# Kernel tuning notes

Measured on AMD Instinct MI355X. Metric: run time of the kernel, lower is better.

Reference implementation:

```python
import jax, jax.numpy as jnp
import numpy as np

N, L, S, D, HD, FC = 4, 2048, 2048, 256, 256, 8  # batch, query len, source len, in_depth, hidden_depth, heads
EPS = 1e-12  # F.normalize eps


def setup_inputs() -> dict:
    key = jax.random.key(0)
    ks = jax.random.split(key, 8)
    sc = 0.05
    return {
        "x0": jax.random.normal(ks[0], (N, L, D), jnp.float32),
        "x1": jax.random.normal(ks[1], (N, S, D), jnp.float32),
        "W0": jax.random.normal(ks[2], (D, HD), jnp.float32) * sc,
        "b0": jax.random.normal(ks[3], (HD,), jnp.float32) * sc,
        "W1": jax.random.normal(ks[4], (D, 2 * HD), jnp.float32) * sc,
        "b1": jax.random.normal(ks[5], (2 * HD,), jnp.float32) * sc,
        "Wm": jax.random.normal(ks[6], (HD, D), jnp.float32) * sc,
        "bm": jax.random.normal(ks[7], (D,), jnp.float32) * sc,
        "alpha": jnp.ones((1,), jnp.float32),
        "beta": jnp.zeros((1,), jnp.float32),
    }


def _l2norm(x):
    # F.normalize(dim=2): x / max(||x||, eps)
    return x / jnp.maximum(jnp.linalg.norm(x, axis=2, keepdims=True), EPS)


def reference(x0, x1, W0, b0, W1, b1, Wm, bm, alpha, beta):
    n, l, _ = x0.shape
    s = x1.shape[1]
    fc = FC
    m = n * fc
    # projections + head split: 'n l (fc c) -> (n fc) l c'
    x0p = (x0 @ W0 + b0).reshape(n, l, fc, -1).transpose(0, 2, 1, 3).reshape(m, l, -1)
    x1p = (x1 @ W1 + b1).reshape(n, s, fc, -1).transpose(0, 2, 1, 3).reshape(m, s, -1)
    x1_point, x1_value = jnp.split(x1p, 2, axis=2)  # each (m, s, c)
    # cosine similarity (m, l, s)
    sim = jnp.einsum('mlc,msc->mls', _l2norm(x0p), _l2norm(x1_point))
    sim = jax.nn.sigmoid(alpha * sim + beta)
    max_val = jnp.max(sim, axis=2)              # (m, l)
    max_idx = jnp.argmax(sim, axis=2)           # (m, l)
    gathered = jnp.take_along_axis(x1_value, max_idx[:, :, None], axis=1)  # (m, l, c)
    new_x0 = max_val[:, :, None] * gathered
    # '(n fc) l c -> n l (fc c)'
    new_x0 = new_x0.reshape(n, fc, l, -1).transpose(0, 2, 1, 3).reshape(n, l, -1)
    return new_x0 @ Wm + bm
```

## Files before the change

kernel.cpp:

```cpp
#include <hip/hip_runtime.h>
#include <hip/hip_bf16.h>
#include <cmath>

#define NB   4
#define LQ   2048
#define SK   2048
#define DD   256
#define HD   256
#define FC   8
#define CH   32
#define MHEAD 32

#define MARGIN 0.0085f
#define CAP    16

#define KROW 40

typedef float f32x16 __attribute__((ext_vector_type(16)));
typedef float f32x2  __attribute__((ext_vector_type(2)));
typedef short bf16x8 __attribute__((ext_vector_type(8)));
typedef unsigned short ushort8v __attribute__((ext_vector_type(8)));

__device__ inline unsigned short f32_to_bf16_bits(float v) {
    __hip_bfloat16 b = __float2bfloat16(v);
    return __builtin_bit_cast(unsigned short, b);
}
__device__ inline unsigned int ord_encode(float v) {
    unsigned int u = __float_as_uint(v);
    return (u & 0x80000000u) ? ~u : (u | 0x80000000u);
}
__device__ inline float ord_decode(unsigned int e) {
    unsigned int u = (e & 0x80000000u) ? (e & 0x7fffffffu) : ~e;
    return __uint_as_float(u);
}

#define MFMA32(a, b, c) __builtin_amdgcn_mfma_f32_32x32x16_bf16(a, b, c, 0, 0, 0)

__global__ __launch_bounds__(256, 7)
void proj_gemm_kernel(const float* __restrict__ x0, const float* __restrict__ x1,
                      const float* __restrict__ W0, const float* __restrict__ b0f,
                      const float* __restrict__ W1, const float* __restrict__ b1f,
                      float* __restrict__ xq, float* __restrict__ xk)
{
    __shared__ float As[2][16][68];
    __shared__ float Bs[2][16][64];
    const int nt  = blockIdx.x;
    const bool is0 = (nt < 4);
    const float* A    = is0 ? x0 : x1;
    const float* B    = is0 ? W0 : W1;
    const float* bias = is0 ? b0f : b1f;
    float* dst        = is0 ? xq : xk;
    const int NB_ = is0 ? HD : 2 * HD;
    const int hw  = is0 ? 32 : 64;
    const int bm  = blockIdx.y * 64;
    const int K   = DD;

    const int tx = threadIdx.x & 15;
    const int ty = threadIdx.x >> 4;
    f32x2 acc2[4][2] = {};

    const int arow = threadIdx.x >> 2;
    const int akq  = (threadIdx.x & 3) << 2;
    const int bkr  = threadIdx.x >> 4;
    const int bnq  = (threadIdx.x & 15) << 2;
    const int fl   = (nt & 3) * 2 + (bnq >> 5);
    const int bcol = fl * hw + (bnq & 31);

    {
        const float4 a4 = *(const float4*)&A[(size_t)(bm + arow) * K + akq];
        const float4 b4 = *(const float4*)&B[(size_t)bkr * NB_ + bcol];
        As[0][akq + 0][arow] = a4.x;
        As[0][akq + 1][arow] = a4.y;
        As[0][akq + 2][arow] = a4.z;
        As[0][akq + 3][arow] = a4.w;
        *(float4*)&Bs[0][bkr][bnq] = b4;
    }
    __syncthreads();

    const int nchunk = K >> 4;
    float4 pa, pb;
    for (int c = 0; c < nchunk; ++c) {
        const int cur = c & 1;
        if (c + 1 < nchunk) {
            const int k0 = (c + 1) << 4;
            pa = *(const float4*)&A[(size_t)(bm + arow) * K + k0 + akq];
            pb = *(const float4*)&B[(size_t)(k0 + bkr) * NB_ + bcol];
        }
        #pragma unroll
        for (int kk = 0; kk < 16; ++kk) {
            const float4 a4 = *(const float4*)&As[cur][kk][ty << 2];
            const float4 bv = *(const float4*)&Bs[cur][kk][tx << 2];
            const f32x2 b01 = {bv.x, bv.y};
            const f32x2 b23 = {bv.z, bv.w};
            const float av[4] = {a4.x, a4.y, a4.z, a4.w};
            #pragma unroll
            for (int i = 0; i < 4; ++i) {
                const f32x2 aa = {av[i], av[i]};
                acc2[i][0] = __builtin_elementwise_fma(aa, b01, acc2[i][0]);
                acc2[i][1] = __builtin_elementwise_fma(aa, b23, acc2[i][1]);
            }
        }
        if (c + 1 < nchunk) {
            const int nxt = cur ^ 1;
            As[nxt][akq + 0][arow] = pa.x;
            As[nxt][akq + 1][arow] = pa.y;
            As[nxt][akq + 2][arow] = pa.z;
            As[nxt][akq + 3][arow] = pa.w;
            *(float4*)&Bs[nxt][bkr][bnq] = pb;
        }
        __syncthreads();
    }

    #pragma unroll
    for (int i = 0; i < 4; ++i) {
        const int row = bm + (ty << 2) + i;
        const int n = row >> 11, l = row & 2047;
        #pragma unroll
        for (int j = 0; j < 4; ++j) {
            const int cl = (tx << 2) + j;
            const int f  = (nt & 3) * 2 + (cl >> 5);
            const int cc = cl & 31;
            const float v = acc2[i][j >> 1][j & 1] + bias[f * hw + cc];
            dst[((((size_t)n * FC + f) * LQ) + l) * CH + cc] = v;
        }
    }
}

__global__ __launch_bounds__(256)
void prep_kernel(const float* __restrict__ x1, const float* __restrict__ Wm,
                 const float* __restrict__ W1,
                 unsigned short* __restrict__ x1b,
                 unsigned short* __restrict__ wm_s,
                 unsigned short* __restrict__ wv_s)
{
    const int i = blockIdx.x * 256 + threadIdx.x;
    if (i < 262144) {
        const float4 a = *(const float4*)(x1 + (size_t)i * 8);
        const float4 b = *(const float4*)(x1 + (size_t)i * 8 + 4);
        ushort8v o;
        o[0] = f32_to_bf16_bits(a.x); o[1] = f32_to_bf16_bits(a.y);
        o[2] = f32_to_bf16_bits(a.z); o[3] = f32_to_bf16_bits(a.w);
        o[4] = f32_to_bf16_bits(b.x); o[5] = f32_to_bf16_bits(b.y);
        o[6] = f32_to_bf16_bits(b.z); o[7] = f32_to_bf16_bits(b.w);
        *(ushort8v*)(x1b + (size_t)i * 8) = o;
    } else if (i < 262144 + 65536) {
        const int j = i - 262144;
        const int k = j >> 8, n = j & 255;
        wm_s[(k >> 4) * 4096 + n * 16 + (k & 15)] = f32_to_bf16_bits(Wm[k * 256 + n]);
    } else {
        const int j = i - 327680;
        const int k = j >> 8, v = j & 255;
        const int w = (v >> 5) * 64 + 32 + (v & 31);
        wv_s[(k >> 4) * 4096 + v * 16 + (k & 15)] = f32_to_bf16_bits(W1[k * 512 + w]);
    }
}

__global__ __launch_bounds__(256)
void val_gemm_kernel(const unsigned short* __restrict__ x1b,
                     const unsigned short* __restrict__ wv_s,
                     const float* __restrict__ b1f, float* __restrict__ xv)
{
    const int wave = threadIdx.x >> 6;
    const int lane = threadIdx.x & 63;
    const int idx  = blockIdx.x * 4 + wave;
    const int mt   = idx >> 3;
    const int nt   = idx & 7;
    const int col  = lane & 31;
    const int g8   = (lane >> 5) * 8;

    const unsigned short* aptr = x1b + (size_t)(mt * 32 + col) * 256 + g8;
    const unsigned short* bptr = wv_s + nt * 32 * 16 + col * 16 + g8;

    f32x16 acc = {0.f, 0.f, 0.f, 0.f, 0.f, 0.f, 0.f, 0.f,
                  0.f, 0.f, 0.f, 0.f, 0.f, 0.f, 0.f, 0.f};
    #pragma unroll 4
    for (int kc = 0; kc < 16; ++kc) {
        const bf16x8 a = *(const bf16x8*)(aptr + kc * 16);
        const bf16x8 bfr = *(const bf16x8*)(bptr + (size_t)kc * 4096);
        acc = MFMA32(a, bfr, acc);
    }

    const int v = nt * 32 + col;
    const int f = v >> 5, c = v & 31;
    const float bias = b1f[f * 64 + 32 + c];
    #pragma unroll
    for (int r = 0; r < 16; ++r) {
        const int g = mt * 32 + (r & 3) + 8 * (r >> 2) + 4 * (lane >> 5);
        const int n = g >> 11, s = g & 2047;
        xv[((((size_t)n * FC + f) * SK) + s) * CH + c] = acc[r] + bias;
    }
}

__global__ __launch_bounds__(256)
void norm_split_init_kernel(float* __restrict__ xq, unsigned short* __restrict__ qhi,
                            float* __restrict__ xk, unsigned short* __restrict__ khi,
                            const float* __restrict__ alpha,
                            unsigned int* __restrict__ maxhh_u, int* __restrict__ cnt)
{
    int r = blockIdx.x * blockDim.x + threadIdx.x;
    float* p;
    unsigned short* dhi;
    float sgn = 1.f;
    if (r < MHEAD * LQ) {
        maxhh_u[r] = 0u;
        cnt[r] = 0;
        p   = xq + (size_t)r * CH;
        dhi = qhi + (size_t)r * CH;
        if (alpha[0] < 0.f) sgn = -1.f;
    } else {
        r -= MHEAD * LQ;
        p   = xk + (size_t)r * CH;
        dhi = khi + (size_t)r * CH;
    }

    float4 v[8];
    float ss = 0.f;
    #pragma unroll
    for (int i = 0; i < 8; ++i) {
        v[i] = *(const float4*)(p + i * 4);
        ss = fmaf(v[i].x, v[i].x, ss);
        ss = fmaf(v[i].y, v[i].y, ss);
        ss = fmaf(v[i].z, v[i].z, ss);
        ss = fmaf(v[i].w, v[i].w, ss);
    }
    const float inv = sgn / fmaxf(sqrtf(ss), 1e-12f);

    ushort8v hb[4];
    #pragma unroll
    for (int i = 0; i < 8; ++i) {
        float4 w;
        w.x = v[i].x * inv; w.y = v[i].y * inv;
        w.z = v[i].z * inv; w.w = v[i].w * inv;
        *(float4*)(p + i * 4) = w;
        hb[i >> 1][(i & 1) * 4 + 0] = f32_to_bf16_bits(w.x);
        hb[i >> 1][(i & 1) * 4 + 1] = f32_to_bf16_bits(w.y);
        hb[i >> 1][(i & 1) * 4 + 2] = f32_to_bf16_bits(w.z);
        hb[i >> 1][(i & 1) * 4 + 3] = f32_to_bf16_bits(w.w);
    }
    #pragma unroll
    for (int i = 0; i < 4; ++i)
        *(ushort8v*)(dhi + i * 8) = hb[i];
}

__global__ __launch_bounds__(256, 4)
void maxpass_kernel(const unsigned short* __restrict__ qhi,
                    const unsigned short* __restrict__ khi,
                    unsigned int* __restrict__ maxhh_u)
{
    __shared__ unsigned short kbuf[2][128 * KROW];
    const int b    = blockIdx.x;
    const int sc   = b & 3;
    const int qb   = (b >> 2) & 15;
    const int h    = b >> 6;
    const int wave = threadIdx.x >> 6;
    const int lane = threadIdx.x & 63;
    const int t    = threadIdx.x;
    const int qbase = qb * 128 + wave * 32;
    const int col   = lane & 31;
    const int g8    = (lane >> 5) * 8;

    const size_t qoff = ((size_t)h * LQ + qbase + col) * CH + g8;
    const bf16x8 ah0 = *(const bf16x8*)(qhi + qoff);
    const bf16x8 ah1 = *(const bf16x8*)(qhi + qoff + 16);

    const unsigned short* kh = khi + ((size_t)h * SK + sc * 512) * CH;

    const int srow  = t >> 1;
    const int shalf = (t & 1) * 16;
    const unsigned short* sp = kh + (size_t)srow * CH + shalf;

    float maxv[16];
    #pragma unroll
    for (int r = 0; r < 16; ++r) maxv[r] = -INFINITY;

    bf16x8 s0 = *(const bf16x8*)(sp);
    bf16x8 s1 = *(const bf16x8*)(sp + 8);
    *(bf16x8*)(&kbuf[0][srow * KROW + shalf])     = s0;
    *(bf16x8*)(&kbuf[0][srow * KROW + shalf + 8]) = s1;
    __syncthreads();

    for (int g = 0; g < 4; ++g) {
        if (g < 3) {
            const unsigned short* spn = sp + (size_t)(g + 1) * 128 * CH;
            s0 = *(const bf16x8*)(spn);
            s1 = *(const bf16x8*)(spn + 8);
        }
        const unsigned short* kbp = &kbuf[g & 1][0];
        #pragma unroll
        for (int tt = 0; tt < 4; ++tt) {
            const int rl = tt * 32 + col;
            const bf16x8 ka  = *(const bf16x8*)(kbp + rl * KROW + g8);
            const bf16x8 kbv = *(const bf16x8*)(kbp + rl * KROW + 16 + g8);
            f32x16 c = {0.f, 0.f, 0.f, 0.f, 0.f, 0.f, 0.f, 0.f,
                        0.f, 0.f, 0.f, 0.f, 0.f, 0.f, 0.f, 0.f};
            c = MFMA32(ah0, ka, c);
            c = MFMA32(ah1, kbv, c);
            #pragma unroll
            for (int r = 0; r < 16; ++r) maxv[r] = fmaxf(maxv[r], c[r]);
        }
        if (g < 3) {
            unsigned short* swn = &kbuf[(g + 1) & 1][srow * KROW + shalf];
            *(bf16x8*)(swn)     = s0;
            *(bf16x8*)(swn + 8) = s1;
            __syncthreads();
        }
    }

    #pragma unroll
    for (int r = 0; r < 16; ++r) {
        float v = maxv[r];
        #pragma unroll
        for (int m = 16; m >= 1; m >>= 1)
            v = fmaxf(v, __shfl_xor(v, m, 64));
        maxv[r] = v;
    }
    if (col == 0) {
        const int rbase = h * LQ + qbase + 4 * (lane >> 5);
        #pragma unroll
        for (int r = 0; r < 16; ++r)
            atomicMax(&maxhh_u[rbase + (r & 3) + 8 * (r >> 2)], ord_encode(maxv[r]));
    }
}

__global__ __launch_bounds__(256, 4)
void candpass_kernel(const unsigned short* __restrict__ qhi,
                     const unsigned short* __restrict__ khi,
                     const unsigned int* __restrict__ maxhh_u,
                     int* __restrict__ cnt, int* __restrict__ cand)
{
    __shared__ unsigned short kbuf[2][128 * KROW];
    const int b    = blockIdx.x;
    const int sc   = b & 3;
    const int qb   = (b >> 2) & 15;
    const int h    = b >> 6;
    const int wave = threadIdx.x >> 6;
    const int lane = threadIdx.x & 63;
    const int t    = threadIdx.x;
    const int qbase = qb * 128 + wave * 32;
    const int col   = lane & 31;
    const int g8    = (lane >> 5) * 8;

    const size_t qoff = ((size_t)h * LQ + qbase + col) * CH + g8;
    const bf16x8 ah0 = *(const bf16x8*)(qhi + qoff);
    const bf16x8 ah1 = *(const bf16x8*)(qhi + qoff + 16);

    int   rows[16];
    float thr[16];
    {
        const int rbase = h * LQ + qbase + 4 * (lane >> 5);
        #pragma unroll
        for (int r = 0; r < 16; ++r) {
            rows[r] = rbase + (r & 3) + 8 * (r >> 2);
            thr[r]  = ord_decode(maxhh_u[rows[r]]) - MARGIN;
        }
    }

    const unsigned short* kh = khi + ((size_t)h * SK + sc * 512) * CH;
    const int sbase = sc * 512;

    const int srow  = t >> 1;
    const int shalf = (t & 1) * 16;
    const unsigned short* sp = kh + (size_t)srow * CH + shalf;

    bf16x8 s0 = *(const bf16x8*)(sp);
    bf16x8 s1 = *(const bf16x8*)(sp + 8);
    *(bf16x8*)(&kbuf[0][srow * KROW + shalf])     = s0;
    *(bf16x8*)(&kbuf[0][srow * KROW + shalf + 8]) = s1;
    __syncthreads();

    for (int g = 0; g < 4; ++g) {
        if (g < 3) {
            const unsigned short* spn = sp + (size_t)(g + 1) * 128 * CH;
            s0 = *(const bf16x8*)(spn);
            s1 = *(const bf16x8*)(spn + 8);
        }
        const unsigned short* kbp = &kbuf[g & 1][0];
        #pragma unroll
        for (int tt = 0; tt < 4; ++tt) {
            const int rl = tt * 32 + col;
            const bf16x8 ka  = *(const bf16x8*)(kbp + rl * KROW + g8);
            const bf16x8 kbv = *(const bf16x8*)(kbp + rl * KROW + 16 + g8);
            f32x16 c = {0.f, 0.f, 0.f, 0.f, 0.f, 0.f, 0.f, 0.f,
                        0.f, 0.f, 0.f, 0.f, 0.f, 0.f, 0.f, 0.f};
            c = MFMA32(ah0, ka, c);
            c = MFMA32(ah1, kbv, c);

            unsigned int hit = 0u;
            #pragma unroll
            for (int r = 0; r < 16; ++r)
                hit = (c[r] >= thr[r]) ? (hit | (1u << r)) : hit;
            if (hit) {
                const int s = sbase + g * 128 + tt * 32 + col;
                #pragma unroll
                for (int r = 0; r < 16; ++r) {
                    if (hit & (1u << r)) {
                        const int slot = atomicAdd(&cnt[rows[r]], 1);
                        if (slot < CAP) cand[(size_t)rows[r] * CAP + slot] = s;
                    }
                }
            }
        }
        if (g < 3) {
            unsigned short* swn = &kbuf[(g + 1) & 1][srow * KROW + shalf];
            *(bf16x8*)(swn)     = s0;
            *(bf16x8*)(swn + 8) = s1;
            __syncthreads();
        }
    }
}

__global__ __launch_bounds__(256)
void refine_gather_kernel(const float* __restrict__ qn,
                          const float* __restrict__ kn,
                          const int* __restrict__ cnt, const int* __restrict__ cand,
                          const float* __restrict__ xv,
                          const float* __restrict__ alpha, const float* __restrict__ beta,
                          unsigned short* __restrict__ nxb)
{
    const int r = blockIdx.x * blockDim.x + threadIdx.x;
    const int h = r >> 11, l = r & 2047;

    float qr[CH];
    #pragma unroll
    for (int i = 0; i < 8; ++i) {
        const float4 v = *(const float4*)(qn + (size_t)r * CH + i * 4);
        qr[i * 4 + 0] = v.x; qr[i * 4 + 1] = v.y;
        qr[i * 4 + 2] = v.z; qr[i * 4 + 3] = v.w;
    }

    int m = cnt[r];
    if (m > CAP) m = CAP;
    float best = -INFINITY;
    int   bidx = 0x7fffffff;
    for (int j = 0; j < m; ++j) {
        const int s = cand[(size_t)r * CAP + j];
        const float4* k4 = (const float4*)(kn + ((size_t)h * SK + s) * CH);
        float p = 0.f;
        #pragma unroll
        for (int c = 0; c < 8; ++c) {
            const float4 kv = k4[c];
            p = fmaf(qr[c * 4 + 0], kv.x, p);
            p = fmaf(qr[c * 4 + 1], kv.y, p);
            p = fmaf(qr[c * 4 + 2], kv.z, p);
            p = fmaf(qr[c * 4 + 3], kv.w, p);
        }
        if (p > best || (p == best && s < bidx)) { best = p; bidx = s; }
    }
    if (bidx == 0x7fffffff) bidx = 0;

    const float a = alpha[0], be = beta[0];
    float tv;
    int idx = bidx;
    if (a == 0.f) { idx = 0; tv = be; }
    else          { tv = fmaf(fabsf(a), best, be); }
    float val;
    if (tv >= 0.f) val = 1.f / (1.f + expf(-tv));
    else           { const float e = expf(tv); val = e / (1.f + e); }

    const float4* vr = (const float4*)(xv + ((size_t)h * SK + idx) * CH);
    const int n = h >> 3, f = h & 7;
    unsigned short* out = nxb + (((size_t)n * LQ + l) * (FC * CH)) + f * CH;
    #pragma unroll
    for (int i = 0; i < 8; ++i) {
        const float4 w = vr[i];
        ushort8v o;
        o[0] = f32_to_bf16_bits(w.x * val);
        o[1] = f32_to_bf16_bits(w.y * val);
        o[2] = f32_to_bf16_bits(w.z * val);
        o[3] = f32_to_bf16_bits(w.w * val);
        *(unsigned long long*)(out + i * 4) = __builtin_bit_cast(unsigned long long,
            *(const ulong1*)&o);
    }
}

__global__ __launch_bounds__(256)
void gemm_out_mfma_kernel(const unsigned short* __restrict__ nxb,
                          const unsigned short* __restrict__ wm_s,
                          const float* __restrict__ bm, float* __restrict__ out)
{
    const int wave = threadIdx.x >> 6;
    const int lane = threadIdx.x & 63;
    const int idx  = blockIdx.x * 4 + wave;
    const int mt   = idx >> 3;
    const int nt   = idx & 7;
    const int col  = lane & 31;
    const int g8   = (lane >> 5) * 8;

    const unsigned short* aptr = nxb + (size_t)(mt * 32 + col) * 256 + g8;
    const unsigned short* bptr = wm_s + nt * 32 * 16 + col * 16 + g8;

    f32x16 acc = {0.f, 0.f, 0.f, 0.f, 0.f, 0.f, 0.f, 0.f,
                  0.f, 0.f, 0.f, 0.f, 0.f, 0.f, 0.f, 0.f};
    #pragma unroll 4
    for (int kc = 0; kc < 16; ++kc) {
        const bf16x8 a = *(const bf16x8*)(aptr + kc * 16);
        const bf16x8 bfr = *(const bf16x8*)(bptr + (size_t)kc * 4096);
        acc = MFMA32(a, bfr, acc);
    }

    const int n0 = nt * 32;
    const float bias = bm[n0 + col];
    #pragma unroll
    for (int r = 0; r < 16; ++r) {
        const int row = mt * 32 + (r & 3) + 8 * (r >> 2) + 4 * (lane >> 5);
        out[(size_t)row * 256 + n0 + col] = acc[r] + bias;
    }
}

extern "C" void kernel_launch(void* const* d_in, const int* in_sizes, int n_in,
                              void* d_out, int out_size, void* d_ws, size_t ws_size,
                              hipStream_t stream)
{
    const float* x0 = (const float*)d_in[0];
    const float* x1 = (const float*)d_in[1];
    const float* W0 = (const float*)d_in[2];
    const float* b0 = (const float*)d_in[3];
    const float* W1 = (const float*)d_in[4];
    const float* b1 = (const float*)d_in[5];
    const float* Wm = (const float*)d_in[6];
    const float* bm = (const float*)d_in[7];
    const float* alpha = (const float*)d_in[8];
    const float* beta  = (const float*)d_in[9];
    float* out = (float*)d_out;

    char* ws = (char*)d_ws;
    const size_t MB = 1024ull * 1024ull;
    float* x0q = (float*)(ws + 0);
    float* x1k = (float*)(ws + 8 * MB);
    float* x1v = (float*)(ws + 16 * MB);
    unsigned short* qhi = (unsigned short*)(ws + 24 * MB);
    unsigned short* khi = (unsigned short*)(ws + 28 * MB);
    unsigned short* x1b = (unsigned short*)(ws + 32 * MB);
    int* cand = (int*)(ws + 32 * MB);
    unsigned int* maxhh_u = (unsigned int*)(ws + 36 * MB);
    int* cnt  = (int*)(ws + 36 * MB + 256 * 1024);
    unsigned short* wm_s = (unsigned short*)(ws + 36 * MB + 512 * 1024);
    unsigned short* wv_s = (unsigned short*)(ws + 36 * MB + 640 * 1024);
    unsigned short* nxb  = (unsigned short*)(ws + 24 * MB);

    const int Mrows = NB * LQ;

    proj_gemm_kernel<<<dim3(8, Mrows / 64), 256, 0, stream>>>(
        x0, x1, W0, b0, W1, b1, x0q, x1k);
    prep_kernel<<<1536, 256, 0, stream>>>(x1, Wm, W1, x1b, wm_s, wv_s);
    val_gemm_kernel<<<512, 256, 0, stream>>>(x1b, wv_s, b1, x1v);
    norm_split_init_kernel<<<(2 * MHEAD * LQ) / 256, 256, 0, stream>>>(
        x0q, qhi, x1k, khi, alpha, maxhh_u, cnt);
    maxpass_kernel<<<2048, 256, 0, stream>>>(qhi, khi, maxhh_u);
    candpass_kernel<<<2048, 256, 0, stream>>>(qhi, khi, maxhh_u, cnt, cand);
    refine_gather_kernel<<<(MHEAD * LQ) / 256, 256, 0, stream>>>(
        x0q, x1k, cnt, cand, x1v, alpha, beta, nxb);
    gemm_out_mfma_kernel<<<512, 256, 0, stream>>>(nxb, wm_s, bm, out);
}
```

Measured before the change: 134.8 us.

## Fuse L2-normalization into projection GEMM epilogue and enlarge max/cand blocks

Removes the separate norm_split_init kernel. The projection GEMM now stages its output tile in shared memory and normalizes each 32-wide head row in the epilogue, writing both the fp32 and bf16 copies. The maxhh/cnt zeroing moves into prep_kernel. maxpass and candpass switch to 512-thread blocks covering 256 queries each, so every K tile loaded to LDS is reused by twice as many waves. The costs are a serialized epilogue in which only 128 threads do the normalization, and a larger shared/register footprint per block.

```diff
diff --git a/kernel.cpp b/kernel.cpp
--- a/kernel.cpp
+++ b/kernel.cpp
@@ -40,16 +40,20 @@
 void proj_gemm_kernel(const float* __restrict__ x0, const float* __restrict__ x1,
                       const float* __restrict__ W0, const float* __restrict__ b0f,
                       const float* __restrict__ W1, const float* __restrict__ b1f,
-                      float* __restrict__ xq, float* __restrict__ xk)
-{
-    __shared__ float As[2][16][68];
-    __shared__ float Bs[2][16][64];
+                      const float* __restrict__ alpha,
+                      float* __restrict__ xq, float* __restrict__ xk,
+                      unsigned short* __restrict__ qhi, unsigned short* __restrict__ khi)
+{
+    __shared__ float SH[4224];
+    #define AS(bf,k,m) SH[(bf)*1088 + (k)*68 + (m)]
+    #define BS(bf,k,n) SH[2176 + (bf)*1024 + (k)*64 + (n)]
     const int nt  = blockIdx.x;
     const bool is0 = (nt < 4);
     const float* A    = is0 ? x0 : x1;
     const float* B    = is0 ? W0 : W1;
     const float* bias = is0 ? b0f : b1f;
-    float* dst        = is0 ? xq : xk;
+    float* dst              = is0 ? xq : xk;
+    unsigned short* dhi     = is0 ? qhi : khi;
     const int NB_ = is0 ? HD : 2 * HD;
     const int hw  = is0 ? 32 : 64;
     const int bm  = blockIdx.y * 64;
@@ -69,11 +73,11 @@
     {
         const float4 a4 = *(const float4*)&A[(size_t)(bm + arow) * K + akq];
         const float4 b4 = *(const float4*)&B[(size_t)bkr * NB_ + bcol];
-        As[0][akq + 0][arow] = a4.x;
-        As[0][akq + 1][arow] = a4.y;
-        As[0][akq + 2][arow] = a4.z;
-        As[0][akq + 3][arow] = a4.w;
-        *(float4*)&Bs[0][bkr][bnq] = b4;
+        AS(0, akq + 0, arow) = a4.x;
+        AS(0, akq + 1, arow) = a4.y;
+        AS(0, akq + 2, arow) = a4.z;
+        AS(0, akq + 3, arow) = a4.w;
+        *(float4*)&BS(0, bkr, bnq) = b4;
     }
     __syncthreads();
 
@@ -88,8 +92,8 @@
         }
         #pragma unroll
         for (int kk = 0; kk < 16; ++kk) {
-            const float4 a4 = *(const float4*)&As[cur][kk][ty << 2];
-            const float4 bv = *(const float4*)&Bs[cur][kk][tx << 2];
+            const float4 a4 = *(const float4*)&AS(cur, kk, ty << 2);
+            const float4 bv = *(const float4*)&BS(cur, kk, tx << 2);
             const f32x2 b01 = {bv.x, bv.y};
             const f32x2 b23 = {bv.z, bv.w};
             const float av[4] = {a4.x, a4.y, a4.z, a4.w};
@@ -102,28 +106,66 @@
         }
         if (c + 1 < nchunk) {
             const int nxt = cur ^ 1;
-            As[nxt][akq + 0][arow] = pa.x;
-            As[nxt][akq + 1][arow] = pa.y;
-            As[nxt][akq + 2][arow] = pa.z;
-            As[nxt][akq + 3][arow] = pa.w;
-            *(float4*)&Bs[nxt][bkr][bnq] = pb;
+            AS(nxt, akq + 0, arow) = pa.x;
+            AS(nxt, akq + 1, arow) = pa.y;
+            AS(nxt, akq + 2, arow) = pa.z;
+            AS(nxt, akq + 3, arow) = pa.w;
+            *(float4*)&BS(nxt, bkr, bnq) = pb;
         }
         __syncthreads();
     }
 
     #pragma unroll
     for (int i = 0; i < 4; ++i) {
-        const int row = bm + (ty << 2) + i;
-        const int n = row >> 11, l = row & 2047;
+        const int row = (ty << 2) + i;
         #pragma unroll
         for (int j = 0; j < 4; ++j) {
             const int cl = (tx << 2) + j;
             const int f  = (nt & 3) * 2 + (cl >> 5);
-            const int cc = cl & 31;
-            const float v = acc2[i][j >> 1][j & 1] + bias[f * hw + cc];
-            dst[((((size_t)n * FC + f) * LQ) + l) * CH + cc] = v;
-        }
-    }
+            SH[row * 66 + cl] = acc2[i][j >> 1][j & 1] + bias[f * hw + (cl & 31)];
+        }
+    }
+    __syncthreads();
+    if (threadIdx.x < 128) {
+        const int row  = threadIdx.x >> 1;
+        const int half = threadIdx.x & 1;
+        const float* src = SH + row * 66 + half * 32;
+        float x[32];
+        float ss = 0.f;
+        #pragma unroll
+        for (int c = 0; c < 32; ++c) {
+            x[c] = src[c];
+            ss = fmaf(x[c], x[c], ss);
+        }
+        float sgn = 1.f;
+        if (is0 && alpha[0] < 0.f) sgn = -1.f;
+        const float inv = sgn / fmaxf(sqrtf(ss), 1e-12f);
+        const int grow = bm + row;
+        const int n = grow >> 11, l = grow & 2047;
+        const int f = (nt & 3) * 2 + half;
+        const size_t off = ((((size_t)n * FC + f) * LQ) + l) * CH;
+        float* df = dst + off;
+        unsigned short* dh = dhi + off;
+        #pragma unroll
+        for (int c4 = 0; c4 < 8; ++c4) {
+            float4 w;
+            w.x = x[c4 * 4 + 0] * inv;
+            w.y = x[c4 * 4 + 1] * inv;
+            w.z = x[c4 * 4 + 2] * inv;
+            w.w = x[c4 * 4 + 3] * inv;
+            *(float4*)(df + c4 * 4) = w;
+        }
+        #pragma unroll
+        for (int c8 = 0; c8 < 4; ++c8) {
+            ushort8v o;
+            #pragma unroll
+            for (int j = 0; j < 8; ++j)
+                o[j] = f32_to_bf16_bits(x[c8 * 8 + j] * inv);
+            *(ushort8v*)(dh + c8 * 8) = o;
+        }
+    }
+    #undef AS
+    #undef BS
 }
 
 __global__ __launch_bounds__(256)
@@ -131,7 +173,8 @@
                  const float* __restrict__ W1,
                  unsigned short* __restrict__ x1b,
                  unsigned short* __restrict__ wm_s,
-                 unsigned short* __restrict__ wv_s)
+                 unsigned short* __restrict__ wv_s,
+                 unsigned int* __restrict__ maxhh_u, int* __restrict__ cnt)
 {
     const int i = blockIdx.x * 256 + threadIdx.x;
     if (i < 262144) {
@@ -143,15 +186,19 @@
         o[4] = f32_to_bf16_bits(b.x); o[5] = f32_to_bf16_bits(b.y);
         o[6] = f32_to_bf16_bits(b.z); o[7] = f32_to_bf16_bits(b.w);
         *(ushort8v*)(x1b + (size_t)i * 8) = o;
-    } else if (i < 262144 + 65536) {
+    } else if (i < 327680) {
         const int j = i - 262144;
         const int k = j >> 8, n = j & 255;
         wm_s[(k >> 4) * 4096 + n * 16 + (k & 15)] = f32_to_bf16_bits(Wm[k * 256 + n]);
-    } else {
+    } else if (i < 393216) {
         const int j = i - 327680;
         const int k = j >> 8, v = j & 255;
         const int w = (v >> 5) * 64 + 32 + (v & 31);
         wv_s[(k >> 4) * 4096 + v * 16 + (k & 15)] = f32_to_bf16_bits(W1[k * 512 + w]);
+    } else if (i < 458752) {
+        maxhh_u[i - 393216] = 0u;
+    } else {
+        cnt[i - 458752] = 0;
     }
 }
 
@@ -191,58 +238,7 @@
     }
 }
 
-__global__ __launch_bounds__(256)
-void norm_split_init_kernel(float* __restrict__ xq, unsigned short* __restrict__ qhi,
-                            float* __restrict__ xk, unsigned short* __restrict__ khi,
-                            const float* __restrict__ alpha,
-                            unsigned int* __restrict__ maxhh_u, int* __restrict__ cnt)
-{
-    int r = blockIdx.x * blockDim.x + threadIdx.x;
-    float* p;
-    unsigned short* dhi;
-    float sgn = 1.f;
-    if (r < MHEAD * LQ) {
-        maxhh_u[r] = 0u;
-        cnt[r] = 0;
-        p   = xq + (size_t)r * CH;
-        dhi = qhi + (size_t)r * CH;
-        if (alpha[0] < 0.f) sgn = -1.f;
-    } else {
-        r -= MHEAD * LQ;
-        p   = xk + (size_t)r * CH;
-        dhi = khi + (size_t)r * CH;
-    }
-
-    float4 v[8];
-    float ss = 0.f;
-    #pragma unroll
-    for (int i = 0; i < 8; ++i) {
-        v[i] = *(const float4*)(p + i * 4);
-        ss = fmaf(v[i].x, v[i].x, ss);
-        ss = fmaf(v[i].y, v[i].y, ss);
-        ss = fmaf(v[i].z, v[i].z, ss);
-        ss = fmaf(v[i].w, v[i].w, ss);
-    }
-    const float inv = sgn / fmaxf(sqrtf(ss), 1e-12f);
-
-    ushort8v hb[4];
-    #pragma unroll
-    for (int i = 0; i < 8; ++i) {
-        float4 w;
-        w.x = v[i].x * inv; w.y = v[i].y * inv;
-        w.z = v[i].z * inv; w.w = v[i].w * inv;
-        *(float4*)(p + i * 4) = w;
-        hb[i >> 1][(i & 1) * 4 + 0] = f32_to_bf16_bits(w.x);
-        hb[i >> 1][(i & 1) * 4 + 1] = f32_to_bf16_bits(w.y);
-        hb[i >> 1][(i & 1) * 4 + 2] = f32_to_bf16_bits(w.z);
-        hb[i >> 1][(i & 1) * 4 + 3] = f32_to_bf16_bits(w.w);
-    }
-    #pragma unroll
-    for (int i = 0; i < 4; ++i)
-        *(ushort8v*)(dhi + i * 8) = hb[i];
-}
-
-__global__ __launch_bounds__(256, 4)
+__global__ __launch_bounds__(512, 4)
 void maxpass_kernel(const unsigned short* __restrict__ qhi,
                     const unsigned short* __restrict__ khi,
                     unsigned int* __restrict__ maxhh_u)
@@ -250,12 +246,12 @@
     __shared__ unsigned short kbuf[2][128 * KROW];
     const int b    = blockIdx.x;
     const int sc   = b & 3;
-    const int qb   = (b >> 2) & 15;
-    const int h    = b >> 6;
-    const int wave = threadIdx.x >> 6;
-    const int lane = threadIdx.x & 63;
+    const int qb   = (b >> 2) & 7;
+    const int h    = b >> 5;
     const int t    = threadIdx.x;
-    const int qbase = qb * 128 + wave * 32;
+    const int wave = t >> 6;
+    const int lane = t & 63;
+    const int qbase = qb * 256 + wave * 32;
     const int col   = lane & 31;
     const int g8    = (lane >> 5) * 8;
 
@@ -265,26 +261,20 @@
 
     const unsigned short* kh = khi + ((size_t)h * SK + sc * 512) * CH;
 
-    const int srow  = t >> 1;
-    const int shalf = (t & 1) * 16;
-    const unsigned short* sp = kh + (size_t)srow * CH + shalf;
+    const int srow = t >> 2;
+    const int sq   = (t & 3) * 8;
+    const unsigned short* sp = kh + (size_t)srow * CH + sq;
 
     float maxv[16];
     #pragma unroll
     for (int r = 0; r < 16; ++r) maxv[r] = -INFINITY;
 
     bf16x8 s0 = *(const bf16x8*)(sp);
-    bf16x8 s1 = *(const bf16x8*)(sp + 8);
-    *(bf16x8*)(&kbuf[0][srow * KROW + shalf])     = s0;
-    *(bf16x8*)(&kbuf[0][srow * KROW + shalf + 8]) = s1;
+    *(bf16x8*)(&kbuf[0][srow * KROW + sq]) = s0;
     __syncthreads();
 
     for (int g = 0; g < 4; ++g) {
-        if (g < 3) {
-            const unsigned short* spn = sp + (size_t)(g + 1) * 128 * CH;
-            s0 = *(const bf16x8*)(spn);
-            s1 = *(const bf16x8*)(spn + 8);
-        }
+        if (g < 3) s0 = *(const bf16x8*)(sp + (size_t)(g + 1) * 128 * CH);
         const unsigned short* kbp = &kbuf[g & 1][0];
         #pragma unroll
         for (int tt = 0; tt < 4; ++tt) {
@@ -299,9 +289,7 @@
             for (int r = 0; r < 16; ++r) maxv[r] = fmaxf(maxv[r], c[r]);
         }
         if (g < 3) {
-            unsigned short* swn = &kbuf[(g + 1) & 1][srow * KROW + shalf];
-            *(bf16x8*)(swn)     = s0;
-            *(bf16x8*)(swn + 8) = s1;
+            *(bf16x8*)(&kbuf[(g + 1) & 1][srow * KROW + sq]) = s0;
             __syncthreads();
         }
     }
@@ -322,7 +310,7 @@
     }
 }
 
-__global__ __launch_bounds__(256, 4)
+__global__ __launch_bounds__(512, 4)
 void candpass_kernel(const unsigned short* __restrict__ qhi,
                      const unsigned short* __restrict__ khi,
                      const unsigned int* __restrict__ maxhh_u,
@@ -331,12 +319,12 @@
     __shared__ unsigned short kbuf[2][128 * KROW];
     const int b    = blockIdx.x;
     const int sc   = b & 3;
-    const int qb   = (b >> 2) & 15;
-    const int h    = b >> 6;
-    const int wave = threadIdx.x >> 6;
-    const int lane = threadIdx.x & 63;
+    const int qb   = (b >> 2) & 7;
+    const int h    = b >> 5;
     const int t    = threadIdx.x;
-    const int qbase = qb * 128 + wave * 32;
+    const int wave = t >> 6;
+    const int lane = t & 63;
+    const int qbase = qb * 256 + wave * 32;
     const int col   = lane & 31;
     const int g8    = (lane >> 5) * 8;
 
@@ -358,22 +346,16 @@
     const unsigned short* kh = khi + ((size_t)h * SK + sc * 512) * CH;
     const int sbase = sc * 512;
 
-    const int srow  = t >> 1;
-    const int shalf = (t & 1) * 16;
-    const unsigned short* sp = kh + (size_t)srow * CH + shalf;
+    const int srow = t >> 2;
+    const int sq   = (t & 3) * 8;
+    const unsigned short* sp = kh + (size_t)srow * CH + sq;
 
     bf16x8 s0 = *(const bf16x8*)(sp);
-    bf16x8 s1 = *(const bf16x8*)(sp + 8);
-    *(bf16x8*)(&kbuf[0][srow * KROW + shalf])     = s0;
-    *(bf16x8*)(&kbuf[0][srow * KROW + shalf + 8]) = s1;
+    *(bf16x8*)(&kbuf[0][srow * KROW + sq]) = s0;
     __syncthreads();
 
     for (int g = 0; g < 4; ++g) {
-        if (g < 3) {
-            const unsigned short* spn = sp + (size_t)(g + 1) * 128 * CH;
-            s0 = *(const bf16x8*)(spn);
-            s1 = *(const bf16x8*)(spn + 8);
-        }
+        if (g < 3) s0 = *(const bf16x8*)(sp + (size_t)(g + 1) * 128 * CH);
         const unsigned short* kbp = &kbuf[g & 1][0];
         #pragma unroll
         for (int tt = 0; tt < 4; ++tt) {
@@ -401,9 +383,7 @@
             }
         }
         if (g < 3) {
-            unsigned short* swn = &kbuf[(g + 1) & 1][srow * KROW + shalf];
-            *(bf16x8*)(swn)     = s0;
-            *(bf16x8*)(swn + 8) = s1;
+            *(bf16x8*)(&kbuf[(g + 1) & 1][srow * KROW + sq]) = s0;
             __syncthreads();
         }
     }
@@ -541,13 +521,11 @@
     const int Mrows = NB * LQ;
 
     proj_gemm_kernel<<<dim3(8, Mrows / 64), 256, 0, stream>>>(
-        x0, x1, W0, b0, W1, b1, x0q, x1k);
-    prep_kernel<<<1536, 256, 0, stream>>>(x1, Wm, W1, x1b, wm_s, wv_s);
+        x0, x1, W0, b0, W1, b1, alpha, x0q, x1k, qhi, khi);
+    prep_kernel<<<2048, 256, 0, stream>>>(x1, Wm, W1, x1b, wm_s, wv_s, maxhh_u, cnt);
     val_gemm_kernel<<<512, 256, 0, stream>>>(x1b, wv_s, b1, x1v);
-    norm_split_init_kernel<<<(2 * MHEAD * LQ) / 256, 256, 0, stream>>>(
-        x0q, qhi, x1k, khi, alpha, maxhh_u, cnt);
-    maxpass_kernel<<<2048, 256, 0, stream>>>(qhi, khi, maxhh_u);
-    candpass_kernel<<<2048, 256, 0, stream>>>(qhi, khi, maxhh_u, cnt, cand);
+    maxpass_kernel<<<1024, 512, 0, stream>>>(qhi, khi, maxhh_u);
+    candpass_kernel<<<1024, 512, 0, stream>>>(qhi, khi, maxhh_u, cnt, cand);
     refine_gather_kernel<<<(MHEAD * LQ) / 256, 256, 0, stream>>>(
         x0q, x1k, cnt, cand, x1v, alpha, beta, nxb);
     gemm_out_mfma_kernel<<<512, 256, 0, stream>>>(nxb, wm_s, bm, out);
```

Measured after the change: 135.9 us. Within noise of the previous version (+0.8%).
